# Kernel tuning notes

Measured on AMD Instinct MI355X. Metric: run time of the kernel, lower is better.

## Reference

```python
import jax, jax.numpy as jnp
import numpy as np

D_MODEL = 256
N_HEADS = 8
NUM_POINTS = [4, 4, 4]
SHAPES = [(80, 80), (40, 40), (20, 20)]
OFFSET_SCALE = 0.5


def _bilinear_sample(val_flat, grid, H, W):
    # val_flat: [BN, H*W, hd]; grid: [BN, Lq, P, 2] in [-1, 1]
    gx, gy = grid[..., 0], grid[..., 1]
    ix = ((gx + 1.0) * W - 1.0) * 0.5
    iy = ((gy + 1.0) * H - 1.0) * 0.5
    ix0 = jnp.floor(ix).astype(jnp.int32)
    iy0 = jnp.floor(iy).astype(jnp.int32)
    ix1, iy1 = ix0 + 1, iy0 + 1
    fx = (ix - ix0)[..., None]
    fy = (iy - iy0)[..., None]

    def valid(xi, yi):
        return ((xi >= 0) & (xi < W) & (yi >= 0) & (yi < H)).astype(val_flat.dtype)[..., None]

    def gather(xi, yi):
        idx = jnp.clip(yi, 0, H - 1) * W + jnp.clip(xi, 0, W - 1)  # [BN, Lq, P]
        BN, Lq, P = idx.shape
        g = jnp.take_along_axis(val_flat, idx.reshape(BN, Lq * P)[:, :, None], axis=1)
        return g.reshape(BN, Lq, P, -1)

    v00 = gather(ix0, iy0) * valid(ix0, iy0)
    v01 = gather(ix1, iy0) * valid(ix1, iy0)
    v10 = gather(ix0, iy1) * valid(ix0, iy1)
    v11 = gather(ix1, iy1) * valid(ix1, iy1)
    return ((1 - fx) * (1 - fy) * v00 + fx * (1 - fy) * v01
            + (1 - fx) * fy * v10 + fx * fy * v11)  # [BN, Lq, P, hd]


def _forward(query, reference_points, input_flatten, W_off, b_off, W_attn, b_attn):
    B, Lq, _ = query.shape
    hd = D_MODEL // N_HEADS
    total = sum(NUM_POINTS)
    value = input_flatten.reshape(B, -1, N_HEADS, hd)  # [B, S, nh, hd]

    off = (query @ W_off + b_off).reshape(B, Lq, N_HEADS, total, 2)
    attn = jax.nn.softmax((query @ W_attn + b_attn).reshape(B, Lq, N_HEADS, total), axis=-1)

    pscale = jnp.concatenate([jnp.full((p,), 1.0 / p, query.dtype) for p in NUM_POINTS])
    # reference_points: [B, Lq, 1, 4] -> broadcast over heads & points
    ref_xy = reference_points[:, :, None, :, :2]   # [B, Lq, 1, 1, 2]
    ref_wh = reference_points[:, :, None, :, 2:]   # [B, Lq, 1, 1, 2]
    loc = ref_xy + off * pscale[None, None, None, :, None] * ref_wh * OFFSET_SCALE

    BN = B * N_HEADS
    val = value.transpose(0, 2, 1, 3).reshape(BN, -1, hd)             # [BN, S, hd]
    grids = (2.0 * loc - 1.0).transpose(0, 2, 1, 3, 4).reshape(BN, Lq, total, 2)

    sizes = [h * w for h, w in SHAPES]
    vals = jnp.split(val, list(np.cumsum(sizes))[:-1], axis=1)
    gs = jnp.split(grids, list(np.cumsum(NUM_POINTS))[:-1], axis=2)
    sampled = jnp.concatenate(
        [_bilinear_sample(v, g, H, W) for v, g, (H, W) in zip(vals, gs, SHAPES)],
        axis=2)  # [BN, Lq, total, hd]

    a = attn.transpose(0, 2, 1, 3).reshape(BN, Lq, total)[..., None]
    out = jnp.sum(sampled * a, axis=2)  # [BN, Lq, hd]
    return out.reshape(B, N_HEADS, Lq, hd).transpose(0, 2, 1, 3).reshape(B, Lq, D_MODEL)


def setup_inputs() -> dict:
    key = jax.random.key(0)
    ks = jax.random.split(key, 5)
    B, Lq, S = 32, 300, sum(h * w for h, w in SHAPES)
    total = sum(NUM_POINTS)
    return {
        'query': jax.random.normal(ks[0], (B, Lq, D_MODEL), jnp.float32),
        'reference_points': jax.random.uniform(ks[1], (B, Lq, 1, 4), jnp.float32),
        'input_flatten': jax.random.normal(ks[2], (B, S, D_MODEL), jnp.float32),
        'W_off': jax.random.normal(ks[3], (D_MODEL, N_HEADS * total * 2), jnp.float32) * 0.02,
        'b_off': jnp.zeros((N_HEADS * total * 2,), jnp.float32),
        'W_attn': jax.random.normal(ks[4], (D_MODEL, N_HEADS * total), jnp.float32) * 0.02,
        'b_attn': jnp.zeros((N_HEADS * total,), jnp.float32),
    }


def reference(query, reference_points, input_flatten, W_off, b_off, W_attn, b_attn):
    return _forward(query, reference_points, input_flatten, W_off, b_off, W_attn, b_attn)
```

## Files before the change

### kernel.cpp

```cpp
#include <hip/hip_runtime.h>

#define NB    32
#define LQ    300
#define DM    256
#define NH    8
#define HD    32
#define NPTS  12
#define NCOLS 288
#define STOT  8400
#define QB    8
#define NBQ   (NB * LQ)
#define NBLK  (NBQ / QB)

static __device__ __forceinline__ float bf2f(unsigned short u) {
    union { unsigned int i; float f; } v;
    v.i = ((unsigned int)u) << 16;
    return v.f;
}

static __device__ __forceinline__ bool vote_f32(const void* p, int t) {
    const unsigned short u = ((const unsigned short*)p)[2 * t];
    const unsigned int e = (u >> 7) & 0xFFu;
    const bool bad = !(u == 0 || (e >= 0x60u && e <= 0x85u));
    return __popcll(__ballot(bad)) >= 16;
}

template<bool WF32>
static __device__ __forceinline__ void proj_cols(
    const void* __restrict__ Wo, const void* __restrict__ bo,
    const void* __restrict__ Wa, const void* __restrict__ ba,
    const float* __restrict__ q_lds, float* __restrict__ proj_lds, int tid)
{
    for (int j = tid; j < NCOLS; j += 256) {
        const void* Wp; const void* bp; int stride, jj;
        if (j < 192) { Wp = Wo; bp = bo; stride = 192; jj = j; }
        else         { Wp = Wa; bp = ba; stride = 96;  jj = j - 192; }

        float acc[QB];
#pragma unroll
        for (int q = 0; q < QB; ++q) acc[q] = 0.f;

        for (int k = 0; k < DM; k += 4) {
            float w[4];
#pragma unroll
            for (int kk = 0; kk < 4; ++kk) {
                const int wi = (k + kk) * stride + jj;
                w[kk] = WF32 ? ((const float*)Wp)[wi]
                             : bf2f(((const unsigned short*)Wp)[wi]);
            }
#pragma unroll
            for (int q = 0; q < QB; ++q) {
                const float4 qv = *(const float4*)&q_lds[q * DM + k];
                acc[q] = fmaf(qv.x, w[0],
                         fmaf(qv.y, w[1],
                         fmaf(qv.z, w[2],
                         fmaf(qv.w, w[3], acc[q]))));
            }
        }

        const float bias = WF32 ? ((const float*)bp)[jj]
                                : bf2f(((const unsigned short*)bp)[jj]);
#pragma unroll
        for (int q = 0; q < QB; ++q)
            proj_lds[q * NCOLS + j] = acc[q] + bias;
    }
}

template<bool VF32>
static __device__ __forceinline__ void sample_tasks(
    const void* __restrict__ value, const float* __restrict__ proj_lds,
    const float* __restrict__ ref_lds, float2* __restrict__ out,
    int q0, int tid)
{
#pragma unroll
    for (int it = 0; it < (QB * 128) / 256; ++it) {
        const int task = it * 256 + tid;
        const int q = task >> 7;
        const int h = (task >> 4) & 7;
        const int l = task & 15;
        const int bq = q0 + q;
        const int b  = bq / LQ;
        const float* pr = proj_lds + q * NCOLS;

        float a[NPTS];
#pragma unroll
        for (int p = 0; p < NPTS; ++p) a[p] = pr[192 + h * NPTS + p];
        float m = a[0];
#pragma unroll
        for (int p = 1; p < NPTS; ++p) m = fmaxf(m, a[p]);
        float s = 0.f;
#pragma unroll
        for (int p = 0; p < NPTS; ++p) { a[p] = __expf(a[p] - m); s += a[p]; }
        const float inv = 1.f / s;

        const float rx = ref_lds[q * 4 + 0];
        const float ry = ref_lds[q * 4 + 1];
        const float rw = ref_lds[q * 4 + 2];
        const float rh = ref_lds[q * 4 + 3];

        const size_t base_e = (size_t)b * STOT * DM + h * HD + l * 2;
        const unsigned int* vb16 = (const unsigned int*)value + (base_e >> 1);
        const float2*       vb32 = (const float2*)value + (base_e >> 1);

        float acc0 = 0.f, acc1 = 0.f;

#pragma unroll
        for (int p = 0; p < NPTS; ++p) {
            const int lvl  = p >> 2;
            const int W    = (lvl == 0) ? 80 : (lvl == 1 ? 40 : 20);
            const int base = (lvl == 0) ? 0  : (lvl == 1 ? 6400 : 8000);

            const float ox = pr[h * 24 + p * 2 + 0];
            const float oy = pr[h * 24 + p * 2 + 1];
            const float ix = (rx + ox * 0.125f * rw) * (float)W - 0.5f;
            const float iy = (ry + oy * 0.125f * rh) * (float)W - 0.5f;

            const float fx0 = floorf(ix), fy0 = floorf(iy);
            const int x0 = (int)fx0, y0 = (int)fy0;
            const float fx = ix - fx0, fy = iy - fy0;
            const float aw = a[p] * inv;

            const float w00 = aw * (1.f - fx) * (1.f - fy);
            const float w01 = aw * fx * (1.f - fy);
            const float w10 = aw * (1.f - fx) * fy;
            const float w11 = aw * fx * fy;

#pragma unroll
            for (int cnr = 0; cnr < 4; ++cnr) {
                const int x = x0 + (cnr & 1);
                const int y = y0 + (cnr >> 1);
                const float wgt = (cnr == 0) ? w00 : (cnr == 1) ? w01
                                 : (cnr == 2) ? w10 : w11;
                const int xc = min(max(x, 0), W - 1);
                const int yc = min(max(y, 0), W - 1);
                const bool ok = (x >= 0) & (x < W) & (y >= 0) & (y < W);
                const float wg = ok ? wgt : 0.f;
                const size_t cell = (size_t)(base + yc * W + xc) * (DM / 2);
                if (VF32) {
                    const float2 v = vb32[cell];
                    acc0 += wg * v.x;
                    acc1 += wg * v.y;
                } else {
                    const unsigned int v = vb16[cell];
                    acc0 += wg * bf2f((unsigned short)(v & 0xffffu));
                    acc1 += wg * bf2f((unsigned short)(v >> 16));
                }
            }
        }

        out[(size_t)bq * (DM / 2) + h * (HD / 2) + l] = make_float2(acc0, acc1);
    }
}

__global__ __launch_bounds__(256) void msda_fused(
    const void* __restrict__ query, const void* __restrict__ refp,
    const void* __restrict__ value, const void* __restrict__ Wo,
    const void* __restrict__ bo,    const void* __restrict__ Wa,
    const void* __restrict__ ba,    float2* __restrict__ out)
{
    __shared__ __align__(16) float q_lds[QB * DM];
    __shared__ float proj_lds[QB * NCOLS];
    __shared__ float ref_lds[QB * 4];
    __shared__ int s_flags;

    const int tid = threadIdx.x;
    const int q0  = blockIdx.x * QB;

    if (tid < 64) {
        int f = 0;
        if (vote_f32(query, tid)) f |= 1;
        if (vote_f32(refp,  tid)) f |= 2;
        if (vote_f32(value, tid)) f |= 4;
        if (vote_f32(Wo,    tid)) f |= 8;
        if (tid == 0) s_flags = f;
    }
    __syncthreads();
    const int fl = s_flags;

    if (fl & 1) {
        for (int i = tid; i < QB * DM; i += 256)
            q_lds[i] = ((const float*)query)[q0 * DM + i];
    } else {
        for (int i = tid; i < QB * DM; i += 256)
            q_lds[i] = bf2f(((const unsigned short*)query)[q0 * DM + i]);
    }
    if (tid < QB * 4) {
        ref_lds[tid] = (fl & 2) ? ((const float*)refp)[q0 * 4 + tid]
                                : bf2f(((const unsigned short*)refp)[q0 * 4 + tid]);
    }
    __syncthreads();

    if (fl & 8) proj_cols<true >(Wo, bo, Wa, ba, q_lds, proj_lds, tid);
    else        proj_cols<false>(Wo, bo, Wa, ba, q_lds, proj_lds, tid);
    __syncthreads();

    if (fl & 4) sample_tasks<true >(value, proj_lds, ref_lds, out, q0, tid);
    else        sample_tasks<false>(value, proj_lds, ref_lds, out, q0, tid);
}

extern "C" void kernel_launch(void* const* d_in, const int* in_sizes, int n_in,
                              void* d_out, int out_size, void* d_ws, size_t ws_size,
                              hipStream_t stream) {
    const void* query = d_in[0];
    const void* refp  = d_in[1];
    const void* vflat = d_in[2];
    const void* Woff  = d_in[3];
    const void* boff  = d_in[4];
    const void* Wattn = d_in[5];
    const void* battn = d_in[6];
    float2* out = (float2*)d_out;
    (void)d_ws; (void)ws_size;

    msda_fused<<<dim3(NBLK), dim3(256), 0, stream>>>(
        query, refp, vflat, Woff, boff, Wattn, battn, out);
}
```

Before: 453.8 us.

## Split projection and sampling into two kernels with float4 value gathers

Splits the single fused kernel into a projection kernel (16 queries per block, one thread per output column) and a separate sampling kernel that reads the projections from workspace. The sampler now gives each thread 4 channels and loads them as float4 instead of float2, which halves the number of gather loads per output. The runtime dtype vote and bf16 paths are removed, so fp32 inputs are assumed. In exchange, the projections make an extra round trip through global memory and a second kernel launch is added.

```diff
diff --git a/kernel.cpp b/kernel.cpp
--- a/kernel.cpp
+++ b/kernel.cpp
@@ -4,213 +4,153 @@
 #define LQ    300
 #define DM    256
 #define NH    8
-#define HD    32
 #define NPTS  12
 #define NCOLS 288
 #define STOT  8400
-#define QB    8
 #define NBQ   (NB * LQ)
-#define NBLK  (NBQ / QB)
 
-static __device__ __forceinline__ float bf2f(unsigned short u) {
-    union { unsigned int i; float f; } v;
-    v.i = ((unsigned int)u) << 16;
-    return v.f;
+#define QB1   16
+#define T1    320
+
+__global__ __launch_bounds__(T1) void msda_proj(
+    const float* __restrict__ query,
+    const float* __restrict__ Wo,
+    const float* __restrict__ bo,
+    const float* __restrict__ Wa,
+    const float* __restrict__ ba,
+    float* __restrict__ proj)
+{
+    __shared__ __align__(16) float q_lds[QB1 * DM];
+    const int tid = threadIdx.x;
+    const int q0  = blockIdx.x * QB1;
+
+    for (int i = tid; i < QB1 * DM; i += T1)
+        q_lds[i] = query[(size_t)q0 * DM + i];
+    __syncthreads();
+
+    const int j = tid;
+    if (j >= NCOLS) return;
+
+    const float* Wp; const float* bp; int stride, jj;
+    if (j < 192) { Wp = Wo; bp = bo; stride = 192; jj = j; }
+    else         { Wp = Wa; bp = ba; stride = 96;  jj = j - 192; }
+
+    float acc[QB1];
+#pragma unroll
+    for (int q = 0; q < QB1; ++q) acc[q] = 0.f;
+
+    for (int k = 0; k < DM; k += 4) {
+        float w0 = Wp[(k + 0) * stride + jj];
+        float w1 = Wp[(k + 1) * stride + jj];
+        float w2 = Wp[(k + 2) * stride + jj];
+        float w3 = Wp[(k + 3) * stride + jj];
+#pragma unroll
+        for (int q = 0; q < QB1; ++q) {
+            const float4 qv = *(const float4*)&q_lds[q * DM + k];
+            acc[q] = fmaf(qv.x, w0,
+                     fmaf(qv.y, w1,
+                     fmaf(qv.z, w2,
+                     fmaf(qv.w, w3, acc[q]))));
+        }
+    }
+
+    const float bias = bp[jj];
+#pragma unroll
+    for (int q = 0; q < QB1; ++q)
+        proj[(size_t)(q0 + q) * NCOLS + j] = acc[q] + bias;
 }
 
-static __device__ __forceinline__ bool vote_f32(const void* p, int t) {
-    const unsigned short u = ((const unsigned short*)p)[2 * t];
-    const unsigned int e = (u >> 7) & 0xFFu;
-    const bool bad = !(u == 0 || (e >= 0x60u && e <= 0x85u));
-    return __popcll(__ballot(bad)) >= 16;
-}
+__global__ __launch_bounds__(256, 4) void msda_sample(
+    const float* __restrict__ value,
+    const float* __restrict__ refp,
+    const float* __restrict__ proj,
+    float4* __restrict__ out)
+{
+    const int gid = blockIdx.x * 256 + threadIdx.x;
+    const int bq  = gid >> 6;
+    const int h   = (gid >> 3) & 7;
+    const int l   = gid & 7;
+    const int b   = bq / LQ;
 
-template<bool WF32>
-static __device__ __forceinline__ void proj_cols(
-    const void* __restrict__ Wo, const void* __restrict__ bo,
-    const void* __restrict__ Wa, const void* __restrict__ ba,
-    const float* __restrict__ q_lds, float* __restrict__ proj_lds, int tid)
-{
-    for (int j = tid; j < NCOLS; j += 256) {
-        const void* Wp; const void* bp; int stride, jj;
-        if (j < 192) { Wp = Wo; bp = bo; stride = 192; jj = j; }
-        else         { Wp = Wa; bp = ba; stride = 96;  jj = j - 192; }
+    const float* pr = proj + (size_t)bq * NCOLS;
 
-        float acc[QB];
+    float a[NPTS];
 #pragma unroll
-        for (int q = 0; q < QB; ++q) acc[q] = 0.f;
+    for (int p = 0; p < NPTS; ++p) a[p] = pr[192 + h * NPTS + p];
+    float m = a[0];
+#pragma unroll
+    for (int p = 1; p < NPTS; ++p) m = fmaxf(m, a[p]);
+    float s = 0.f;
+#pragma unroll
+    for (int p = 0; p < NPTS; ++p) { a[p] = __expf(a[p] - m); s += a[p]; }
+    const float inv = 1.f / s;
 
-        for (int k = 0; k < DM; k += 4) {
-            float w[4];
-#pragma unroll
-            for (int kk = 0; kk < 4; ++kk) {
-                const int wi = (k + kk) * stride + jj;
-                w[kk] = WF32 ? ((const float*)Wp)[wi]
-                             : bf2f(((const unsigned short*)Wp)[wi]);
-            }
-#pragma unroll
-            for (int q = 0; q < QB; ++q) {
-                const float4 qv = *(const float4*)&q_lds[q * DM + k];
-                acc[q] = fmaf(qv.x, w[0],
-                         fmaf(qv.y, w[1],
-                         fmaf(qv.z, w[2],
-                         fmaf(qv.w, w[3], acc[q]))));
-            }
-        }
+    const float rx = refp[bq * 4 + 0];
+    const float ry = refp[bq * 4 + 1];
+    const float rw = refp[bq * 4 + 2];
+    const float rh = refp[bq * 4 + 3];
 
-        const float bias = WF32 ? ((const float*)bp)[jj]
-                                : bf2f(((const unsigned short*)bp)[jj]);
-#pragma unroll
-        for (int q = 0; q < QB; ++q)
-            proj_lds[q * NCOLS + j] = acc[q] + bias;
-    }
-}
+    const float4* vb = (const float4*)value + ((size_t)b * STOT * 64 + h * 8 + l);
 
-template<bool VF32>
-static __device__ __forceinline__ void sample_tasks(
-    const void* __restrict__ value, const float* __restrict__ proj_lds,
-    const float* __restrict__ ref_lds, float2* __restrict__ out,
-    int q0, int tid)
-{
-#pragma unroll
-    for (int it = 0; it < (QB * 128) / 256; ++it) {
-        const int task = it * 256 + tid;
-        const int q = task >> 7;
-        const int h = (task >> 4) & 7;
-        const int l = task & 15;
-        const int bq = q0 + q;
-        const int b  = bq / LQ;
-        const float* pr = proj_lds + q * NCOLS;
-
-        float a[NPTS];
-#pragma unroll
-        for (int p = 0; p < NPTS; ++p) a[p] = pr[192 + h * NPTS + p];
-        float m = a[0];
-#pragma unroll
-        for (int p = 1; p < NPTS; ++p) m = fmaxf(m, a[p]);
-        float s = 0.f;
-#pragma unroll
-        for (int p = 0; p < NPTS; ++p) { a[p] = __expf(a[p] - m); s += a[p]; }
-        const float inv = 1.f / s;
-
-        const float rx = ref_lds[q * 4 + 0];
-        const float ry = ref_lds[q * 4 + 1];
-        const float rw = ref_lds[q * 4 + 2];
-        const float rh = ref_lds[q * 4 + 3];
-
-        const size_t base_e = (size_t)b * STOT * DM + h * HD + l * 2;
-        const unsigned int* vb16 = (const unsigned int*)value + (base_e >> 1);
-        const float2*       vb32 = (const float2*)value + (base_e >> 1);
-
-        float acc0 = 0.f, acc1 = 0.f;
+    float ax = 0.f, ay = 0.f, az = 0.f, aw4 = 0.f;
 
 #pragma unroll
-        for (int p = 0; p < NPTS; ++p) {
-            const int lvl  = p >> 2;
-            const int W    = (lvl == 0) ? 80 : (lvl == 1 ? 40 : 20);
-            const int base = (lvl == 0) ? 0  : (lvl == 1 ? 6400 : 8000);
+    for (int p = 0; p < NPTS; ++p) {
+        const int lvl  = p >> 2;
+        const int W    = (lvl == 0) ? 80 : (lvl == 1 ? 40 : 20);
+        const int base = (lvl == 0) ? 0  : (lvl == 1 ? 6400 : 8000);
 
-            const float ox = pr[h * 24 + p * 2 + 0];
-            const float oy = pr[h * 24 + p * 2 + 1];
-            const float ix = (rx + ox * 0.125f * rw) * (float)W - 0.5f;
-            const float iy = (ry + oy * 0.125f * rh) * (float)W - 0.5f;
+        const float ox = pr[h * 24 + p * 2 + 0];
+        const float oy = pr[h * 24 + p * 2 + 1];
+        const float ix = fmaf(fmaf(ox, 0.125f * rw, rx), (float)W, -0.5f);
+        const float iy = fmaf(fmaf(oy, 0.125f * rh, ry), (float)W, -0.5f);
 
-            const float fx0 = floorf(ix), fy0 = floorf(iy);
-            const int x0 = (int)fx0, y0 = (int)fy0;
-            const float fx = ix - fx0, fy = iy - fy0;
-            const float aw = a[p] * inv;
+        const float fx0 = floorf(ix), fy0 = floorf(iy);
+        const int x0 = (int)fx0, y0 = (int)fy0;
+        const float fx = ix - fx0, fy = iy - fy0;
+        const float awt = a[p] * inv;
 
-            const float w00 = aw * (1.f - fx) * (1.f - fy);
-            const float w01 = aw * fx * (1.f - fy);
-            const float w10 = aw * (1.f - fx) * fy;
-            const float w11 = aw * fx * fy;
+        const float w00 = awt * (1.f - fx) * (1.f - fy);
+        const float w01 = awt * fx * (1.f - fy);
+        const float w10 = awt * (1.f - fx) * fy;
+        const float w11 = awt * fx * fy;
 
 #pragma unroll
-            for (int cnr = 0; cnr < 4; ++cnr) {
-                const int x = x0 + (cnr & 1);
-                const int y = y0 + (cnr >> 1);
-                const float wgt = (cnr == 0) ? w00 : (cnr == 1) ? w01
-                                 : (cnr == 2) ? w10 : w11;
-                const int xc = min(max(x, 0), W - 1);
-                const int yc = min(max(y, 0), W - 1);
-                const bool ok = (x >= 0) & (x < W) & (y >= 0) & (y < W);
-                const float wg = ok ? wgt : 0.f;
-                const size_t cell = (size_t)(base + yc * W + xc) * (DM / 2);
-                if (VF32) {
-                    const float2 v = vb32[cell];
-                    acc0 += wg * v.x;
-                    acc1 += wg * v.y;
-                } else {
-                    const unsigned int v = vb16[cell];
-                    acc0 += wg * bf2f((unsigned short)(v & 0xffffu));
-                    acc1 += wg * bf2f((unsigned short)(v >> 16));
-                }
-            }
+        for (int cnr = 0; cnr < 4; ++cnr) {
+            const int x = x0 + (cnr & 1);
+            const int y = y0 + (cnr >> 1);
+            const float wgt = (cnr == 0) ? w00 : (cnr == 1) ? w01
+                             : (cnr == 2) ? w10 : w11;
+            const int xc = min(max(x, 0), W - 1);
+            const int yc = min(max(y, 0), W - 1);
+            const bool ok = (x >= 0) & (x < W) & (y >= 0) & (y < W);
+            const float wg = ok ? wgt : 0.f;
+            const float4 v = vb[(size_t)(base + yc * W + xc) * 64];
+            ax  = fmaf(wg, v.x, ax);
+            ay  = fmaf(wg, v.y, ay);
+            az  = fmaf(wg, v.z, az);
+            aw4 = fmaf(wg, v.w, aw4);
         }
+    }
 
-        out[(size_t)bq * (DM / 2) + h * (HD / 2) + l] = make_float2(acc0, acc1);
-    }
-}
-
-__global__ __launch_bounds__(256) void msda_fused(
-    const void* __restrict__ query, const void* __restrict__ refp,
-    const void* __restrict__ value, const void* __restrict__ Wo,
-    const void* __restrict__ bo,    const void* __restrict__ Wa,
-    const void* __restrict__ ba,    float2* __restrict__ out)
-{
-    __shared__ __align__(16) float q_lds[QB * DM];
-    __shared__ float proj_lds[QB * NCOLS];
-    __shared__ float ref_lds[QB * 4];
-    __shared__ int s_flags;
-
-    const int tid = threadIdx.x;
-    const int q0  = blockIdx.x * QB;
-
-    if (tid < 64) {
-        int f = 0;
-        if (vote_f32(query, tid)) f |= 1;
-        if (vote_f32(refp,  tid)) f |= 2;
-        if (vote_f32(value, tid)) f |= 4;
-        if (vote_f32(Wo,    tid)) f |= 8;
-        if (tid == 0) s_flags = f;
-    }
-    __syncthreads();
-    const int fl = s_flags;
-
-    if (fl & 1) {
-        for (int i = tid; i < QB * DM; i += 256)
-            q_lds[i] = ((const float*)query)[q0 * DM + i];
-    } else {
-        for (int i = tid; i < QB * DM; i += 256)
-            q_lds[i] = bf2f(((const unsigned short*)query)[q0 * DM + i]);
-    }
-    if (tid < QB * 4) {
-        ref_lds[tid] = (fl & 2) ? ((const float*)refp)[q0 * 4 + tid]
-                                : bf2f(((const unsigned short*)refp)[q0 * 4 + tid]);
-    }
-    __syncthreads();
-
-    if (fl & 8) proj_cols<true >(Wo, bo, Wa, ba, q_lds, proj_lds, tid);
-    else        proj_cols<false>(Wo, bo, Wa, ba, q_lds, proj_lds, tid);
-    __syncthreads();
-
-    if (fl & 4) sample_tasks<true >(value, proj_lds, ref_lds, out, q0, tid);
-    else        sample_tasks<false>(value, proj_lds, ref_lds, out, q0, tid);
+    out[(size_t)bq * 64 + h * 8 + l] = make_float4(ax, ay, az, aw4);
 }
 
 extern "C" void kernel_launch(void* const* d_in, const int* in_sizes, int n_in,
                               void* d_out, int out_size, void* d_ws, size_t ws_size,
                               hipStream_t stream) {
-    const void* query = d_in[0];
-    const void* refp  = d_in[1];
-    const void* vflat = d_in[2];
-    const void* Woff  = d_in[3];
-    const void* boff  = d_in[4];
-    const void* Wattn = d_in[5];
-    const void* battn = d_in[6];
-    float2* out = (float2*)d_out;
-    (void)d_ws; (void)ws_size;
+    const float* query = (const float*)d_in[0];
+    const float* refp  = (const float*)d_in[1];
+    const float* vflat = (const float*)d_in[2];
+    const float* Woff  = (const float*)d_in[3];
+    const float* boff  = (const float*)d_in[4];
+    const float* Wattn = (const float*)d_in[5];
+    const float* battn = (const float*)d_in[6];
+    float4* out = (float4*)d_out;
+    float* proj = (float*)d_ws;
 
-    msda_fused<<<dim3(NBLK), dim3(256), 0, stream>>>(
-        query, refp, vflat, Woff, boff, Wattn, battn, out);
+    msda_proj<<<dim3(NBQ / QB1), dim3(T1), 0, stream>>>(
+        query, Woff, boff, Wattn, battn, proj);
+    msda_sample<<<dim3(NBQ * 64 / 256), dim3(256), 0, stream>>>(
+        vflat, refp, proj, out);
 }
```

Result: faster. 423.6 us (-6.7%).
